# Kernel tuning notes

Hardware: AMD Instinct MI355X
Metric: run time of the kernel (lower is better)

Reference implementation:

```python
import jax, jax.numpy as jnp
import numpy as np


def setup_inputs() -> dict:
    key = jax.random.key(0)
    x = jax.random.normal(key, (64_000_000,), dtype=jnp.float32)
    return {"x": x, "num_bins": 64}


def reference(x, num_bins):
    # Faithful translation of Histogram.from_named_array / sharded_histogram.
    a = x.ravel()
    mn = a.min()
    mx = a.max()
    num = jnp.int32(a.size)
    s = a.sum()
    ss = (a * a).sum()
    # jnp.histogram_bin_edges with int bins == linspace(min, max, bins+1)
    edges = mn + (mx - mn) * jnp.linspace(0.0, 1.0, num_bins + 1, dtype=a.dtype)
    # Original does an O(N * num_bins) broadcast compare with HALF-OPEN bins
    # [edges[i], edges[i+1]) for every bin (so elements == max fall in no bin),
    # then adds 1 to the last bucket. digitize computes the identical binning
    # in O(N log num_bins) without the N x num_bins intermediate:
    #   idx = j+1  <=>  edges[j] <= a < edges[j+1];  idx=0 underflow; idx=num_bins+1 overflow (incl. a == max)
    idx = jnp.digitize(a, edges)
    counts_full = jnp.zeros(num_bins + 2, dtype=jnp.int32).at[idx].add(1)
    counts = counts_full[1 : num_bins + 1].at[-1].add(1)
    return mn, mx, num, s, ss, edges, counts
```

## Files before the change

kernel.cpp:

```cpp
#include <hip/hip_runtime.h>
#include <hip/hip_bf16.h>
#include <stdint.h>


__device__ __forceinline__ unsigned fkey(float f) {
    unsigned u = __float_as_uint(f);
    return (u & 0x80000000u) ? ~u : (u | 0x80000000u);
}
__device__ __forceinline__ float funkey(unsigned k) {
    unsigned u = (k & 0x80000000u) ? (k ^ 0x80000000u) : ~k;
    return __uint_as_float(u);
}

__global__ void k_init(unsigned* minkey, unsigned* maxkey,
                       unsigned long long* sfx, unsigned long long* ssfx,
                       unsigned* ghist) {
    int t = threadIdx.x;
    if (t < 64) ghist[t] = 0u;
    if (t == 64) *minkey = 0xFFFFFFFFu;
    if (t == 65) *maxkey = 0u;
    if (t == 66) *sfx = 0ull;
    if (t == 67) *ssfx = 0ull;
}

__global__ __launch_bounds__(256) void k_reduce(
    const float* __restrict__ x, long long n,
    unsigned* __restrict__ ws_minkey, unsigned* __restrict__ ws_maxkey,
    unsigned long long* __restrict__ ws_sfx, unsigned long long* __restrict__ ws_ssfx)
{
    const float4* __restrict__ x4 = (const float4*)x;
    const long long n4 = n >> 2;
    const int lane = threadIdx.x & 63;
    const int wv   = threadIdx.x >> 6;
    const long long gw     = (long long)blockIdx.x * 4 + wv;
    const long long nwaves = (long long)gridDim.x * 4;
    const long long per_iter = nwaves * 512;

    float lmin = INFINITY, lmax = -INFINITY;
    float ls0 = 0.0f, ls1 = 0.0f, lq0 = 0.0f, lq1 = 0.0f;

#define ACC4(v, S, Q) do {                                                 \
        lmin = fminf(lmin, fminf(fminf((v).x, (v).y), fminf((v).z, (v).w))); \
        lmax = fmaxf(lmax, fmaxf(fmaxf((v).x, (v).y), fmaxf((v).z, (v).w))); \
        S += ((v).x + (v).y) + ((v).z + (v).w);                            \
        Q = fmaf((v).x, (v).x, Q); Q = fmaf((v).y, (v).y, Q);              \
        Q = fmaf((v).z, (v).z, Q); Q = fmaf((v).w, (v).w, Q);              \
    } while (0)

    for (long long base = gw * 512; base + 512 <= n4; base += per_iter) {
        const float4* __restrict__ p = x4 + base + lane;
        const float4* __restrict__ q = p + 256;
        float4 a0 = p[0], a1 = p[64], a2 = p[128], a3 = p[192];
        float4 a4 = q[0], a5 = q[64], a6 = q[128], a7 = q[192];
        ACC4(a0, ls0, lq0); ACC4(a1, ls1, lq1);
        ACC4(a2, ls0, lq0); ACC4(a3, ls1, lq1);
        ACC4(a4, ls0, lq0); ACC4(a5, ls1, lq1);
        ACC4(a6, ls0, lq0); ACC4(a7, ls1, lq1);
    }
    {
        const long long rem_start = n4 & ~511LL;
        if (blockIdx.x == 0) {
            for (long long i = rem_start + threadIdx.x; i < n4; i += 256) {
                float4 v = x4[i];
                ACC4(v, ls0, lq0);
            }
        }
    }
#undef ACC4
    if (blockIdx.x == 0 && (long long)threadIdx.x < (n & 3)) {
        float v = x[(n4 << 2) + threadIdx.x];
        lmin = fminf(lmin, v); lmax = fmaxf(lmax, v);
        ls0 += v; lq0 = fmaf(v, v, lq0);
    }
    float ls = ls0 + ls1, lss = lq0 + lq1;
    #pragma unroll
    for (int off = 32; off > 0; off >>= 1) {
        lmin = fminf(lmin, __shfl_down(lmin, off, 64));
        lmax = fmaxf(lmax, __shfl_down(lmax, off, 64));
        ls  += __shfl_down(ls,  off, 64);
        lss += __shfl_down(lss, off, 64);
    }
    __shared__ float smin[4], smax[4], ssum[4], ssq[4];
    if ((threadIdx.x & 63) == 0) {
        smin[wv] = lmin; smax[wv] = lmax; ssum[wv] = ls; ssq[wv] = lss;
    }
    __syncthreads();
    if (threadIdx.x == 0) {
        float bmin = fminf(fminf(smin[0], smin[1]), fminf(smin[2], smin[3]));
        float bmax = fmaxf(fmaxf(smax[0], smax[1]), fmaxf(smax[2], smax[3]));
        float bs   = (ssum[0] + ssum[1]) + (ssum[2] + ssum[3]);
        float bss  = (ssq[0]  + ssq[1])  + (ssq[2]  + ssq[3]);
        atomicMin(ws_minkey, fkey(bmin));
        atomicMax(ws_maxkey, fkey(bmax));
        atomicAdd(ws_sfx,  (unsigned long long)(long long)((double)bs  * 1048576.0));
        atomicAdd(ws_ssfx, (unsigned long long)(long long)((double)bss * 1048576.0));
    }
}

__global__ __launch_bounds__(256) void k_hist(
    const float* __restrict__ x, long long n,
    const unsigned* __restrict__ ws_minkey, const unsigned* __restrict__ ws_maxkey,
    unsigned* __restrict__ ghist)
{
    __shared__ unsigned hl[64 * 64];
    for (int i = threadIdx.x; i < 64 * 64; i += 256) hl[i] = 0u;

    const float mn  = funkey(*ws_minkey);
    const float mx  = funkey(*ws_maxkey);
    const float d   = __fsub_rn(mx, mn);
    const float inv = __fdiv_rn(64.0f, d);
    const float base = -mn * inv;
    __syncthreads();

    const float4* __restrict__ x4 = (const float4*)x;
    const long long n4 = n >> 2;
    const unsigned c = threadIdx.x & 63u;
    const int lane = threadIdx.x & 63;
    const int wv   = threadIdx.x >> 6;
    const long long gw     = (long long)blockIdx.x * 4 + wv;
    const long long nwaves = (long long)gridDim.x * 4;
    const long long per_iter = nwaves * 512;

    auto binup = [&](float4 v) {
        int j0 = (int)fmaf(v.x, inv, base); j0 = j0 > 63 ? 63 : j0;
        int j1 = (int)fmaf(v.y, inv, base); j1 = j1 > 63 ? 63 : j1;
        int j2 = (int)fmaf(v.z, inv, base); j2 = j2 > 63 ? 63 : j2;
        int j3 = (int)fmaf(v.w, inv, base); j3 = j3 > 63 ? 63 : j3;
        atomicAdd(&hl[(unsigned)j0 * 64u + c], 1u);
        atomicAdd(&hl[(unsigned)j1 * 64u + c], 1u);
        atomicAdd(&hl[(unsigned)j2 * 64u + c], 1u);
        atomicAdd(&hl[(unsigned)j3 * 64u + c], 1u);
    };

    for (long long b = gw * 512; b + 512 <= n4; b += per_iter) {
        const float4* __restrict__ p = x4 + b + lane;
        const float4* __restrict__ q = p + 256;
        float4 a0 = p[0], a1 = p[64], a2 = p[128], a3 = p[192];
        float4 a4 = q[0], a5 = q[64], a6 = q[128], a7 = q[192];
        binup(a0); binup(a1); binup(a2); binup(a3);
        binup(a4); binup(a5); binup(a6); binup(a7);
    }
    {
        const long long rem_start = n4 & ~511LL;
        if (blockIdx.x == 0)
            for (long long i = rem_start + threadIdx.x; i < n4; i += 256)
                binup(x4[i]);
    }
    if (blockIdx.x == 0 && (long long)threadIdx.x < (n & 3)) {
        float v = x[(n4 << 2) + threadIdx.x];
        int j = (int)fmaf(v, inv, base); j = j > 63 ? 63 : j;
        atomicAdd(&hl[(unsigned)j * 64u + c], 1u);
    }
    __syncthreads();
    if (threadIdx.x < 64) {
        const unsigned b = threadIdx.x;
        unsigned s = 0;
        #pragma unroll
        for (unsigned k = 0; k < 64; ++k)
            s += hl[b * 64u + ((k + b) & 63u)];
        atomicAdd(&ghist[b], s);
    }
}

__global__ void k_fin(const unsigned* ws_minkey, const unsigned* ws_maxkey,
                      const unsigned long long* ws_sfx, const unsigned long long* ws_ssfx,
                      const unsigned* ghist, float* out, float fnum)
{
    const int t = threadIdx.x;
    const float mn = funkey(*ws_minkey);
    const float mx = funkey(*ws_maxkey);
    const float d  = __fsub_rn(mx, mn);
    if (t == 0) out[0] = mn;
    else if (t == 1) out[1] = mx;
    else if (t == 2) out[2] = fnum;
    else if (t == 3) out[3] = (float)((double)(long long)(*ws_sfx)  * 9.5367431640625e-07);
    else if (t == 4) out[4] = (float)((double)(long long)(*ws_ssfx) * 9.5367431640625e-07);
    else if (t >= 5 && t < 70) {
        int i = t - 5;
        out[t] = __fadd_rn(mn, __fmul_rn(d, (float)i * 0.015625f));
    } else if (t >= 70 && t < 134) {
        int b = t - 70;
        unsigned cv = ghist[b] + (b == 63 ? 1u : 0u);
        out[t] = (float)cv;
    }
}

extern "C" void kernel_launch(void* const* d_in, const int* in_sizes, int n_in,
                              void* d_out, int out_size, void* d_ws, size_t ws_size,
                              hipStream_t stream)
{
    const float* x = (const float*)d_in[0];
    const long long n = (long long)in_sizes[0];

    unsigned* minkey = (unsigned*)d_ws;
    unsigned* maxkey = minkey + 1;
    unsigned long long* sfx  = (unsigned long long*)((char*)d_ws + 8);
    unsigned long long* ssfx = (unsigned long long*)((char*)d_ws + 16);
    unsigned* ghist = (unsigned*)((char*)d_ws + 32);

    k_init<<<1, 128, 0, stream>>>(minkey, maxkey, sfx, ssfx, ghist);

    const int blocks = 2048;
    k_reduce<<<blocks, 256, 0, stream>>>(x, n, minkey, maxkey, sfx, ssfx);
    k_hist<<<blocks, 256, 0, stream>>>(x, n, minkey, maxkey, ghist);
    k_fin<<<1, 192, 0, stream>>>(minkey, maxkey, sfx, ssfx, ghist,
                                 (float*)d_out, (float)n);
}
```

Before: 434.3 us.

## Fuse reduce, histogram and finalize into one persistent kernel with grid barriers

Merges the min/max/sum reduction, histogram and finalize kernels into one kernel launched with 1024 blocks. Blocks sync through atomic-counter grid barriers instead of kernel boundaries. The goal is to cut launch overhead and let the second pass over the 256MB input hit in cache. The barrier assumes all 1024 blocks are co-resident, with a deadlock risk if occupancy is lower, and it halves the grid size.

```diff
diff --git a/kernel.cpp b/kernel.cpp
--- a/kernel.cpp
+++ b/kernel.cpp
@@ -1,5 +1,4 @@
 #include <hip/hip_runtime.h>
-#include <hip/hip_bf16.h>
 #include <stdint.h>
 
 
@@ -12,176 +11,195 @@
     return __uint_as_float(u);
 }
 
+__device__ __forceinline__ void gbar(unsigned* bar, unsigned target) {
+    __syncthreads();
+    if (threadIdx.x == 0) {
+        __hip_atomic_fetch_add(bar, 1u, __ATOMIC_ACQ_REL, __HIP_MEMORY_SCOPE_AGENT);
+        while (__hip_atomic_load(bar, __ATOMIC_ACQUIRE, __HIP_MEMORY_SCOPE_AGENT) < target) {
+            __builtin_amdgcn_s_sleep(16);
+        }
+    }
+    __syncthreads();
+}
+
 __global__ void k_init(unsigned* minkey, unsigned* maxkey,
                        unsigned long long* sfx, unsigned long long* ssfx,
-                       unsigned* ghist) {
+                       unsigned* bar1, unsigned* bar2, unsigned* ghist) {
     int t = threadIdx.x;
     if (t < 64) ghist[t] = 0u;
     if (t == 64) *minkey = 0xFFFFFFFFu;
     if (t == 65) *maxkey = 0u;
     if (t == 66) *sfx = 0ull;
     if (t == 67) *ssfx = 0ull;
-}
-
-__global__ __launch_bounds__(256) void k_reduce(
+    if (t == 68) *bar1 = 0u;
+    if (t == 69) *bar2 = 0u;
+}
+
+__global__ __launch_bounds__(256, 4) void k_main(
     const float* __restrict__ x, long long n,
-    unsigned* __restrict__ ws_minkey, unsigned* __restrict__ ws_maxkey,
-    unsigned long long* __restrict__ ws_sfx, unsigned long long* __restrict__ ws_ssfx)
+    unsigned* minkey, unsigned* maxkey,
+    unsigned long long* sfx, unsigned long long* ssfx,
+    unsigned* bar1, unsigned* bar2,
+    unsigned* ghist, float* out)
 {
+    __shared__ unsigned hl[64 * 64];
+    __shared__ float smin[4], smax[4], ssum[4], ssq[4];
+
+    const int lane = threadIdx.x & 63;
+    const int wv   = threadIdx.x >> 6;
     const float4* __restrict__ x4 = (const float4*)x;
     const long long n4 = n >> 2;
-    const int lane = threadIdx.x & 63;
-    const int wv   = threadIdx.x >> 6;
     const long long gw     = (long long)blockIdx.x * 4 + wv;
     const long long nwaves = (long long)gridDim.x * 4;
     const long long per_iter = nwaves * 512;
-
-    float lmin = INFINITY, lmax = -INFINITY;
-    float ls0 = 0.0f, ls1 = 0.0f, lq0 = 0.0f, lq1 = 0.0f;
-
-#define ACC4(v, S, Q) do {                                                 \
+    const unsigned nblocks = gridDim.x;
+
+    for (int i = threadIdx.x; i < 64 * 64; i += 256) hl[i] = 0u;
+
+    {
+        float lmin = INFINITY, lmax = -INFINITY;
+        float ls0 = 0.0f, ls1 = 0.0f, lq0 = 0.0f, lq1 = 0.0f;
+
+#define ACC4(v, S, Q) do {                                                   \
         lmin = fminf(lmin, fminf(fminf((v).x, (v).y), fminf((v).z, (v).w))); \
         lmax = fmaxf(lmax, fmaxf(fmaxf((v).x, (v).y), fmaxf((v).z, (v).w))); \
-        S += ((v).x + (v).y) + ((v).z + (v).w);                            \
-        Q = fmaf((v).x, (v).x, Q); Q = fmaf((v).y, (v).y, Q);              \
-        Q = fmaf((v).z, (v).z, Q); Q = fmaf((v).w, (v).w, Q);              \
+        S += ((v).x + (v).y) + ((v).z + (v).w);                              \
+        Q = fmaf((v).x, (v).x, Q); Q = fmaf((v).y, (v).y, Q);                \
+        Q = fmaf((v).z, (v).z, Q); Q = fmaf((v).w, (v).w, Q);                \
     } while (0)
 
-    for (long long base = gw * 512; base + 512 <= n4; base += per_iter) {
-        const float4* __restrict__ p = x4 + base + lane;
-        const float4* __restrict__ q = p + 256;
-        float4 a0 = p[0], a1 = p[64], a2 = p[128], a3 = p[192];
-        float4 a4 = q[0], a5 = q[64], a6 = q[128], a7 = q[192];
-        ACC4(a0, ls0, lq0); ACC4(a1, ls1, lq1);
-        ACC4(a2, ls0, lq0); ACC4(a3, ls1, lq1);
-        ACC4(a4, ls0, lq0); ACC4(a5, ls1, lq1);
-        ACC4(a6, ls0, lq0); ACC4(a7, ls1, lq1);
-    }
+        for (long long base = gw * 512; base + 512 <= n4; base += per_iter) {
+            const float4* __restrict__ p = x4 + base + lane;
+            const float4* __restrict__ q = p + 256;
+            float4 a0 = p[0], a1 = p[64], a2 = p[128], a3 = p[192];
+            float4 a4 = q[0], a5 = q[64], a6 = q[128], a7 = q[192];
+            ACC4(a0, ls0, lq0); ACC4(a1, ls1, lq1);
+            ACC4(a2, ls0, lq0); ACC4(a3, ls1, lq1);
+            ACC4(a4, ls0, lq0); ACC4(a5, ls1, lq1);
+            ACC4(a6, ls0, lq0); ACC4(a7, ls1, lq1);
+        }
+        {
+            const long long rem_start = n4 & ~511LL;
+            if (blockIdx.x == 0) {
+                for (long long i = rem_start + threadIdx.x; i < n4; i += 256) {
+                    float4 v = x4[i];
+                    ACC4(v, ls0, lq0);
+                }
+            }
+        }
+#undef ACC4
+        if (blockIdx.x == 0 && (long long)threadIdx.x < (n & 3)) {
+            float v = x[(n4 << 2) + threadIdx.x];
+            lmin = fminf(lmin, v); lmax = fmaxf(lmax, v);
+            ls0 += v; lq0 = fmaf(v, v, lq0);
+        }
+        float ls = ls0 + ls1, lss = lq0 + lq1;
+        #pragma unroll
+        for (int off = 32; off > 0; off >>= 1) {
+            lmin = fminf(lmin, __shfl_down(lmin, off, 64));
+            lmax = fmaxf(lmax, __shfl_down(lmax, off, 64));
+            ls  += __shfl_down(ls,  off, 64);
+            lss += __shfl_down(lss, off, 64);
+        }
+        if ((threadIdx.x & 63) == 0) {
+            smin[wv] = lmin; smax[wv] = lmax; ssum[wv] = ls; ssq[wv] = lss;
+        }
+        __syncthreads();
+        if (threadIdx.x == 0) {
+            float bmin = fminf(fminf(smin[0], smin[1]), fminf(smin[2], smin[3]));
+            float bmax = fmaxf(fmaxf(smax[0], smax[1]), fmaxf(smax[2], smax[3]));
+            float bs   = (ssum[0] + ssum[1]) + (ssum[2] + ssum[3]);
+            float bss  = (ssq[0]  + ssq[1])  + (ssq[2]  + ssq[3]);
+            atomicMin(minkey, fkey(bmin));
+            atomicMax(maxkey, fkey(bmax));
+            atomicAdd(sfx,  (unsigned long long)(long long)((double)bs  * 1048576.0));
+            atomicAdd(ssfx, (unsigned long long)(long long)((double)bss * 1048576.0));
+        }
+    }
+
+    gbar(bar1, nblocks);
+
     {
-        const long long rem_start = n4 & ~511LL;
-        if (blockIdx.x == 0) {
-            for (long long i = rem_start + threadIdx.x; i < n4; i += 256) {
-                float4 v = x4[i];
-                ACC4(v, ls0, lq0);
-            }
-        }
-    }
-#undef ACC4
-    if (blockIdx.x == 0 && (long long)threadIdx.x < (n & 3)) {
-        float v = x[(n4 << 2) + threadIdx.x];
-        lmin = fminf(lmin, v); lmax = fmaxf(lmax, v);
-        ls0 += v; lq0 = fmaf(v, v, lq0);
-    }
-    float ls = ls0 + ls1, lss = lq0 + lq1;
-    #pragma unroll
-    for (int off = 32; off > 0; off >>= 1) {
-        lmin = fminf(lmin, __shfl_down(lmin, off, 64));
-        lmax = fmaxf(lmax, __shfl_down(lmax, off, 64));
-        ls  += __shfl_down(ls,  off, 64);
-        lss += __shfl_down(lss, off, 64);
-    }
-    __shared__ float smin[4], smax[4], ssum[4], ssq[4];
-    if ((threadIdx.x & 63) == 0) {
-        smin[wv] = lmin; smax[wv] = lmax; ssum[wv] = ls; ssq[wv] = lss;
-    }
-    __syncthreads();
-    if (threadIdx.x == 0) {
-        float bmin = fminf(fminf(smin[0], smin[1]), fminf(smin[2], smin[3]));
-        float bmax = fmaxf(fmaxf(smax[0], smax[1]), fmaxf(smax[2], smax[3]));
-        float bs   = (ssum[0] + ssum[1]) + (ssum[2] + ssum[3]);
-        float bss  = (ssq[0]  + ssq[1])  + (ssq[2]  + ssq[3]);
-        atomicMin(ws_minkey, fkey(bmin));
-        atomicMax(ws_maxkey, fkey(bmax));
-        atomicAdd(ws_sfx,  (unsigned long long)(long long)((double)bs  * 1048576.0));
-        atomicAdd(ws_ssfx, (unsigned long long)(long long)((double)bss * 1048576.0));
-    }
-}
-
-__global__ __launch_bounds__(256) void k_hist(
-    const float* __restrict__ x, long long n,
-    const unsigned* __restrict__ ws_minkey, const unsigned* __restrict__ ws_maxkey,
-    unsigned* __restrict__ ghist)
-{
-    __shared__ unsigned hl[64 * 64];
-    for (int i = threadIdx.x; i < 64 * 64; i += 256) hl[i] = 0u;
-
-    const float mn  = funkey(*ws_minkey);
-    const float mx  = funkey(*ws_maxkey);
-    const float d   = __fsub_rn(mx, mn);
-    const float inv = __fdiv_rn(64.0f, d);
-    const float base = -mn * inv;
-    __syncthreads();
-
-    const float4* __restrict__ x4 = (const float4*)x;
-    const long long n4 = n >> 2;
-    const unsigned c = threadIdx.x & 63u;
-    const int lane = threadIdx.x & 63;
-    const int wv   = threadIdx.x >> 6;
-    const long long gw     = (long long)blockIdx.x * 4 + wv;
-    const long long nwaves = (long long)gridDim.x * 4;
-    const long long per_iter = nwaves * 512;
-
-    auto binup = [&](float4 v) {
-        int j0 = (int)fmaf(v.x, inv, base); j0 = j0 > 63 ? 63 : j0;
-        int j1 = (int)fmaf(v.y, inv, base); j1 = j1 > 63 ? 63 : j1;
-        int j2 = (int)fmaf(v.z, inv, base); j2 = j2 > 63 ? 63 : j2;
-        int j3 = (int)fmaf(v.w, inv, base); j3 = j3 > 63 ? 63 : j3;
-        atomicAdd(&hl[(unsigned)j0 * 64u + c], 1u);
-        atomicAdd(&hl[(unsigned)j1 * 64u + c], 1u);
-        atomicAdd(&hl[(unsigned)j2 * 64u + c], 1u);
-        atomicAdd(&hl[(unsigned)j3 * 64u + c], 1u);
-    };
-
-    for (long long b = gw * 512; b + 512 <= n4; b += per_iter) {
-        const float4* __restrict__ p = x4 + b + lane;
-        const float4* __restrict__ q = p + 256;
-        float4 a0 = p[0], a1 = p[64], a2 = p[128], a3 = p[192];
-        float4 a4 = q[0], a5 = q[64], a6 = q[128], a7 = q[192];
-        binup(a0); binup(a1); binup(a2); binup(a3);
-        binup(a4); binup(a5); binup(a6); binup(a7);
-    }
-    {
-        const long long rem_start = n4 & ~511LL;
-        if (blockIdx.x == 0)
-            for (long long i = rem_start + threadIdx.x; i < n4; i += 256)
-                binup(x4[i]);
-    }
-    if (blockIdx.x == 0 && (long long)threadIdx.x < (n & 3)) {
-        float v = x[(n4 << 2) + threadIdx.x];
-        int j = (int)fmaf(v, inv, base); j = j > 63 ? 63 : j;
-        atomicAdd(&hl[(unsigned)j * 64u + c], 1u);
-    }
-    __syncthreads();
-    if (threadIdx.x < 64) {
-        const unsigned b = threadIdx.x;
-        unsigned s = 0;
-        #pragma unroll
-        for (unsigned k = 0; k < 64; ++k)
-            s += hl[b * 64u + ((k + b) & 63u)];
-        atomicAdd(&ghist[b], s);
-    }
-}
-
-__global__ void k_fin(const unsigned* ws_minkey, const unsigned* ws_maxkey,
-                      const unsigned long long* ws_sfx, const unsigned long long* ws_ssfx,
-                      const unsigned* ghist, float* out, float fnum)
-{
-    const int t = threadIdx.x;
-    const float mn = funkey(*ws_minkey);
-    const float mx = funkey(*ws_maxkey);
-    const float d  = __fsub_rn(mx, mn);
-    if (t == 0) out[0] = mn;
-    else if (t == 1) out[1] = mx;
-    else if (t == 2) out[2] = fnum;
-    else if (t == 3) out[3] = (float)((double)(long long)(*ws_sfx)  * 9.5367431640625e-07);
-    else if (t == 4) out[4] = (float)((double)(long long)(*ws_ssfx) * 9.5367431640625e-07);
-    else if (t >= 5 && t < 70) {
-        int i = t - 5;
-        out[t] = __fadd_rn(mn, __fmul_rn(d, (float)i * 0.015625f));
-    } else if (t >= 70 && t < 134) {
-        int b = t - 70;
-        unsigned cv = ghist[b] + (b == 63 ? 1u : 0u);
-        out[t] = (float)cv;
+        const float mn  = funkey(__hip_atomic_load(minkey, __ATOMIC_RELAXED,
+                                                   __HIP_MEMORY_SCOPE_AGENT));
+        const float mx  = funkey(__hip_atomic_load(maxkey, __ATOMIC_RELAXED,
+                                                   __HIP_MEMORY_SCOPE_AGENT));
+        const float d   = __fsub_rn(mx, mn);
+        const float inv = __fdiv_rn(64.0f, d);
+        const float base = -mn * inv;
+        const unsigned c = threadIdx.x & 63u;
+
+        auto binup = [&](float4 v) {
+            int j0 = (int)fmaf(v.x, inv, base); j0 = j0 > 63 ? 63 : j0;
+            int j1 = (int)fmaf(v.y, inv, base); j1 = j1 > 63 ? 63 : j1;
+            int j2 = (int)fmaf(v.z, inv, base); j2 = j2 > 63 ? 63 : j2;
+            int j3 = (int)fmaf(v.w, inv, base); j3 = j3 > 63 ? 63 : j3;
+            atomicAdd(&hl[(unsigned)j0 * 64u + c], 1u);
+            atomicAdd(&hl[(unsigned)j1 * 64u + c], 1u);
+            atomicAdd(&hl[(unsigned)j2 * 64u + c], 1u);
+            atomicAdd(&hl[(unsigned)j3 * 64u + c], 1u);
+        };
+
+        for (long long b = gw * 512; b + 512 <= n4; b += per_iter) {
+            const float4* __restrict__ p = x4 + b + lane;
+            const float4* __restrict__ q = p + 256;
+            float4 a0 = p[0], a1 = p[64], a2 = p[128], a3 = p[192];
+            float4 a4 = q[0], a5 = q[64], a6 = q[128], a7 = q[192];
+            binup(a0); binup(a1); binup(a2); binup(a3);
+            binup(a4); binup(a5); binup(a6); binup(a7);
+        }
+        {
+            const long long rem_start = n4 & ~511LL;
+            if (blockIdx.x == 0)
+                for (long long i = rem_start + threadIdx.x; i < n4; i += 256)
+                    binup(x4[i]);
+        }
+        if (blockIdx.x == 0 && (long long)threadIdx.x < (n & 3)) {
+            float v = x[(n4 << 2) + threadIdx.x];
+            int j = (int)fmaf(v, inv, base); j = j > 63 ? 63 : j;
+            atomicAdd(&hl[(unsigned)j * 64u + c], 1u);
+        }
+        __syncthreads();
+        if (threadIdx.x < 64) {
+            const unsigned b = threadIdx.x;
+            unsigned s = 0;
+            #pragma unroll
+            for (unsigned k = 0; k < 64; ++k)
+                s += hl[b * 64u + ((k + b) & 63u)];
+            atomicAdd(&ghist[b], s);
+        }
+    }
+
+    gbar(bar2, nblocks);
+
+    if (blockIdx.x == 0) {
+        const int t = threadIdx.x;
+        const float mn = funkey(__hip_atomic_load(minkey, __ATOMIC_RELAXED,
+                                                  __HIP_MEMORY_SCOPE_AGENT));
+        const float mx = funkey(__hip_atomic_load(maxkey, __ATOMIC_RELAXED,
+                                                  __HIP_MEMORY_SCOPE_AGENT));
+        const float d  = __fsub_rn(mx, mn);
+        if (t == 0) out[0] = mn;
+        else if (t == 1) out[1] = mx;
+        else if (t == 2) out[2] = (float)n;
+        else if (t == 3) {
+            unsigned long long v = __hip_atomic_load(sfx, __ATOMIC_RELAXED,
+                                                     __HIP_MEMORY_SCOPE_AGENT);
+            out[3] = (float)((double)(long long)v * 9.5367431640625e-07);
+        } else if (t == 4) {
+            unsigned long long v = __hip_atomic_load(ssfx, __ATOMIC_RELAXED,
+                                                     __HIP_MEMORY_SCOPE_AGENT);
+            out[4] = (float)((double)(long long)v * 9.5367431640625e-07);
+        } else if (t >= 5 && t < 70) {
+            int i = t - 5;
+            out[t] = __fadd_rn(mn, __fmul_rn(d, (float)i * 0.015625f));
+        } else if (t >= 70 && t < 134) {
+            int b = t - 70;
+            unsigned cv = __hip_atomic_load(&ghist[b], __ATOMIC_RELAXED,
+                                            __HIP_MEMORY_SCOPE_AGENT)
+                          + (b == 63 ? 1u : 0u);
+            out[t] = (float)cv;
+        }
     }
 }
 
@@ -190,19 +208,19 @@
                               hipStream_t stream)
 {
     const float* x = (const float*)d_in[0];
-    const long long n = (long long)in_sizes[0];
+    long long n = (long long)in_sizes[0];
 
     unsigned* minkey = (unsigned*)d_ws;
     unsigned* maxkey = minkey + 1;
     unsigned long long* sfx  = (unsigned long long*)((char*)d_ws + 8);
     unsigned long long* ssfx = (unsigned long long*)((char*)d_ws + 16);
+    unsigned* bar1 = (unsigned*)((char*)d_ws + 24);
+    unsigned* bar2 = (unsigned*)((char*)d_ws + 28);
     unsigned* ghist = (unsigned*)((char*)d_ws + 32);
-
-    k_init<<<1, 128, 0, stream>>>(minkey, maxkey, sfx, ssfx, ghist);
-
-    const int blocks = 2048;
-    k_reduce<<<blocks, 256, 0, stream>>>(x, n, minkey, maxkey, sfx, ssfx);
-    k_hist<<<blocks, 256, 0, stream>>>(x, n, minkey, maxkey, ghist);
-    k_fin<<<1, 192, 0, stream>>>(minkey, maxkey, sfx, ssfx, ghist,
-                                 (float*)d_out, (float)n);
-}
+    float* out = (float*)d_out;
+
+    k_init<<<1, 128, 0, stream>>>(minkey, maxkey, sfx, ssfx, bar1, bar2, ghist);
+
+    k_main<<<1024, 256, 0, stream>>>(x, n, minkey, maxkey, sfx, ssfx,
+                                     bar1, bar2, ghist, out);
+}
```

Result: slower. 742.5 us (+71.0%).
